# Optimization experiments

Hardware: AMD Instinct MI355X
Metric: run time of the kernel (lower is better)

The kernel has to match this reference:

```python
import jax, jax.numpy as jnp
import numpy as np

EPS = 1e-5

def mvn(x):
    # instance norm per (batch, channel) over spatial, torch var is unbiased (ddof=1)
    b, c, h, w = x.shape
    xf = x.reshape(b, c, h * w)
    mean = xf.mean(axis=2)[:, :, None, None]
    std = jnp.sqrt(jnp.var(xf, axis=2, ddof=1) + EPS)[:, :, None, None]
    return (x - mean) / std

def conv1x1(x, W, b):
    # W: [C_out, C_in], 1x1 conv == channel matmul
    return jnp.einsum('oc,bchw->bohw', W, x) + b[None, :, None, None]

def attention(Fq, G, Hs, mask_map, Wo, bo, hard):
    b, c, h, w = Fq.shape
    N = h * w
    Fm = Fq.reshape(b, c, N)          # [b,c,N]
    Gm = G.reshape(b, c, N)           # [b,c,N]
    S = jnp.einsum('bcn,bcm->bnm', Fm, Gm)  # [b,N,N] scores
    neg = -jnp.finfo(S.dtype).max
    S = jnp.where(mask_map[None, :, :] < 0.5, neg, S)
    if hard:
        # keep only the row-wise argmax entry, everything else -> neg (then softmax)
        idx = jnp.argmax(S, axis=2)                      # [b,N]
        sel = jnp.arange(N)[None, None, :] == idx[:, :, None]
        S = jnp.where(sel, S, neg)
    A = jax.nn.softmax(S, axis=-1)    # [b,N,N]
    Hm = Hs.reshape(b, c, N)
    O = jnp.einsum('bcm,bnm->bcn', Hm, A).reshape(b, c, h, w)
    return conv1x1(O, Wo, bo)

def setup_inputs() -> dict:
    key = jax.random.key(0)
    ks = jax.random.split(key, 16)
    C = 256
    shp = (2, C, 64, 64)
    inp = {
        'content': jax.random.normal(ks[0], shp, jnp.float32),
        'style': jax.random.normal(ks[1], shp, jnp.float32),
        'content_sem': jax.random.normal(ks[2], shp, jnp.float32),
        'style_sem': jax.random.normal(ks[3], shp, jnp.float32),
        'map_32': jax.random.uniform(ks[4], (1024, 1024), jnp.float32),
        'map_64': jax.random.uniform(ks[5], (4096, 4096), jnp.float32),
        't1': 1,
        't2': 1,
        'Wf': jax.random.normal(ks[6], (C, C), jnp.float32) * 0.02,
        'bf': jnp.zeros((C,), jnp.float32),
        'Wg': jax.random.normal(ks[7], (C, C), jnp.float32) * 0.02,
        'bg': jnp.zeros((C,), jnp.float32),
        'Wh': jax.random.normal(ks[8], (C, C), jnp.float32) * 0.02,
        'bh': jnp.zeros((C,), jnp.float32),
        'Wo': jax.random.normal(ks[9], (C, C), jnp.float32) * 0.02,
        'bo': jnp.zeros((C,), jnp.float32),
    }
    return inp

def reference(content, style, content_sem, style_sem, map_32, map_64, t1, t2,
              Wf, bf, Wg, bg, Wh, bh, Wo, bo):
    # h*w == 4096 -> map_64 masking branch is active (static shape decision)
    H_style = conv1x1(style, Wh, bh)
    # SCA: soft attention over semantic features
    x_sca = attention(conv1x1(mvn(content_sem), Wf, bf),
                      conv1x1(mvn(style_sem), Wg, bg),
                      H_style, map_64, Wo, bo, hard=False)
    # SSA: hard-argmax attention over content/style features
    x_ssa = attention(conv1x1(mvn(content), Wf, bf),
                      conv1x1(mvn(style), Wg, bg),
                      H_style, map_64, Wo, bo, hard=True)
    return t1 * x_sca + t2 * x_ssa + content
```

## Files before the change

kernel.cpp:

```cpp
#include <hip/hip_runtime.h>
#include <hip/hip_bf16.h>
#include <cstddef>

typedef unsigned short u16;
typedef unsigned int   u32;
typedef unsigned long long u64;
typedef short v8s __attribute__((ext_vector_type(8)));
typedef u16   v8u __attribute__((ext_vector_type(8)));
typedef float v4f __attribute__((ext_vector_type(4)));

#define CH  256
#define NSP 4096
#define NB  2

__device__ __forceinline__ float b2f(u16 u){ u32 t = ((u32)u) << 16; float f; __builtin_memcpy(&f, &t, 4); return f; }
__device__ __forceinline__ u16 f2b(float f){
  u32 x; __builtin_memcpy(&x, &f, 4);
  u32 r = x + 0x7FFFu + ((x >> 16) & 1u);
  return (u16)(r >> 16);
}
__device__ __forceinline__ u32 f2sortable(float f){
  u32 x; __builtin_memcpy(&x, &f, 4);
  return (x & 0x80000000u) ? ~x : (x | 0x80000000u);
}
__device__ __forceinline__ float sortable2f(u32 u){
  u32 x = (u & 0x80000000u) ? (u ^ 0x80000000u) : ~u;
  float f; __builtin_memcpy(&f, &x, 4);
  return f;
}

__global__ __launch_bounds__(256) void k_stats(
    const float* __restrict__ x0, const float* __restrict__ x1,
    const float* __restrict__ x2, const float* __restrict__ x3,
    float* __restrict__ meanv, float* __restrict__ rstdv){
  int bid = blockIdx.x;
  int t = bid >> 9, row = bid & 511;
  const float* src = (t==0?x0: t==1?x1: t==2?x2: x3) + (size_t)row*NSP;
  int tid = threadIdx.x;
  double sx = 0.0, sq = 0.0;
  const float4* p4 = (const float4*)src;
  #pragma unroll
  for (int k=0;k<4;k++){
    float4 v = p4[tid + k*256];
    double a=v.x,bb=v.y,c=v.z,d=v.w;
    sx += a+bb+c+d;
    sq += a*a + bb*bb + c*c + d*d;
  }
  #pragma unroll
  for (int off=1; off<64; off<<=1){ sx += __shfl_xor(sx, off); sq += __shfl_xor(sq, off); }
  __shared__ double wsx[4], wsq[4];
  int w = tid >> 6;
  if ((tid & 63) == 0){ wsx[w] = sx; wsq[w] = sq; }
  __syncthreads();
  if (tid == 0){
    double SX = wsx[0]+wsx[1]+wsx[2]+wsx[3];
    double SQ = wsq[0]+wsq[1]+wsq[2]+wsq[3];
    double mean = SX / 4096.0;
    double var  = (SQ - 4096.0*mean*mean) / 4095.0;
    double rstd = 1.0 / sqrt(var + 1e-5);
    meanv[bid] = (float)mean;
    rstdv[bid] = (float)rstd;
  }
}

__global__ __launch_bounds__(256) void k_weights(
    const float* __restrict__ Wo, const float* __restrict__ Wh,
    const float* __restrict__ bh, const float* __restrict__ bo,
    u16* __restrict__ W2, float* __restrict__ b2v){
  int o = blockIdx.x, c = threadIdx.x;
  __shared__ float wo[256];
  __shared__ float red[256];
  wo[c] = Wo[o*256 + c];
  __syncthreads();
  float acc = 0.f;
  for (int j=0;j<256;j++) acc += wo[j] * Wh[j*256 + c];
  W2[o*256 + c] = f2b(acc);
  red[c] = wo[c] * bh[c];
  __syncthreads();
  for (int s=128;s>0;s>>=1){ if (c < s) red[c] += red[c+s]; __syncthreads(); }
  if (c == 0) b2v[o] = red[0] + bo[o];
}

__global__ __launch_bounds__(256) void k_maskbits(
    const float* __restrict__ map, u32* __restrict__ bits){
  int wid = blockIdx.x*256 + threadIdx.x;
  const float4* p = (const float4*)(map + (size_t)wid*32);
  u32 m = 0;
  #pragma unroll
  for (int k=0;k<8;k++){
    float4 v = p[k];
    m |= (u32)(v.x >= 0.5f) << (k*4+0);
    m |= (u32)(v.y >= 0.5f) << (k*4+1);
    m |= (u32)(v.z >= 0.5f) << (k*4+2);
    m |= (u32)(v.w >= 0.5f) << (k*4+3);
  }
  bits[wid] = m;
}

__global__ __launch_bounds__(256,2) void k_conv_sca(
    const float* __restrict__ x, const float* __restrict__ W,
    const float* __restrict__ meanv, const float* __restrict__ rstdv, int statBase,
    const float* __restrict__ biasv, u16* __restrict__ outB){
  __shared__ u16 As[64][72];
  __shared__ u16 Bs[64][72];
  int o0 = blockIdx.x*64, n0 = blockIdx.y*64, b = blockIdx.z;
  int tid = threadIdx.x, w = tid>>6, lane = tid&63, col = lane&15, q = lane>>4;
  v4f acc[4] = {};
  int crA = tid>>2, nseg = (tid&3)*16;
  for (int kc=0; kc<4; kc++){
    int cg = kc*64;
    {
      int srow = statBase + b*256 + cg + crA;
      float mean = meanv[srow], rstd = rstdv[srow];
      const float4* xr = (const float4*)(x + ((size_t)(b*256 + cg + crA))*NSP + n0 + nseg);
      #pragma unroll
      for (int k4=0;k4<4;k4++){
        float4 v = xr[k4];
        As[nseg+k4*4+0][crA] = f2b((v.x-mean)*rstd);
        As[nseg+k4*4+1][crA] = f2b((v.y-mean)*rstd);
        As[nseg+k4*4+2][crA] = f2b((v.z-mean)*rstd);
        As[nseg+k4*4+3][crA] = f2b((v.w-mean)*rstd);
      }
    }
    {
      const float4* wr = (const float4*)(W + ((size_t)(o0 + crA))*256 + cg + nseg);
      #pragma unroll
      for (int h=0;h<2;h++){
        float4 a = wr[h*2], c = wr[h*2+1];
        v8u o;
        o[0]=f2b(a.x); o[1]=f2b(a.y); o[2]=f2b(a.z); o[3]=f2b(a.w);
        o[4]=f2b(c.x); o[5]=f2b(c.y); o[6]=f2b(c.z); o[7]=f2b(c.w);
        *(v8u*)&Bs[crA][nseg + h*8] = o;
      }
    }
    __syncthreads();
    #pragma unroll
    for (int ks=0;ks<2;ks++){
      v8s af = *(v8s*)&As[w*16 + col][ks*32 + q*8];
      #pragma unroll
      for (int js=0;js<4;js++){
        v8s bfr = *(v8s*)&Bs[js*16 + col][ks*32 + q*8];
        acc[js] = __builtin_amdgcn_mfma_f32_16x16x32_bf16(af, bfr, acc[js], 0, 0, 0);
      }
    }
    __syncthreads();
  }
  #pragma unroll
  for (int js=0;js<4;js++){
    int o = o0 + js*16 + col;
    float bj = biasv[o];
    #pragma unroll
    for (int reg=0;reg<4;reg++){
      int n = n0 + w*16 + q*4 + reg;
      outB[((size_t)(b*NSP + n))*256 + o] = f2b(acc[js][reg] + bj);
    }
  }
}

__global__ __launch_bounds__(256,2) void k_conv_ssa(
    const float* __restrict__ x, const float* __restrict__ W,
    const float* __restrict__ meanv, const float* __restrict__ rstdv, int statBase,
    const float* __restrict__ biasv,
    float* __restrict__ outF, u16* __restrict__ outB){
  __shared__ u32 As32[64][100];
  __shared__ u32 Bs32[64][100];
  int o0 = blockIdx.x*64, n0 = blockIdx.y*64, b = blockIdx.z;
  int tid = threadIdx.x, w = tid>>6, lane = tid&63, col = lane&15, q = lane>>4;
  v4f acc[4] = {};
  int cA = tid>>3, nnA = (tid&7)*8;
  int oB = tid>>2, cB = (tid&3)*8;
  for (int g=0; g<8; g++){
    int cg = g*32;
    {
      int srow = statBase + b*256 + cg + cA;
      float mean = meanv[srow], rstd = rstdv[srow];
      const float4* xr = (const float4*)(x + ((size_t)(b*256 + cg + cA))*NSP + n0 + nnA);
      float4 v0 = xr[0], v1 = xr[1];
      float xv[8] = {v0.x,v0.y,v0.z,v0.w,v1.x,v1.y,v1.z,v1.w};
      #pragma unroll
      for (int e=0;e<8;e++){
        float xm = (xv[e]-mean)*rstd;
        u16 s0 = f2b(xm);  float r1 = xm - b2f(s0);
        u16 s1 = f2b(r1);  float r2 = r1 - b2f(s1);
        u16 s2 = f2b(r2);
        As32[nnA+e][cA*3+0] = (u32)s0 | ((u32)s1<<16);
        As32[nnA+e][cA*3+1] = (u32)s2 | ((u32)s0<<16);
        As32[nnA+e][cA*3+2] = (u32)s1 | ((u32)s0<<16);
      }
    }
    {
      const float4* wr = (const float4*)(W + ((size_t)(o0 + oB))*256 + cg + cB);
      float4 w0v = wr[0], w1v = wr[1];
      float wv[8] = {w0v.x,w0v.y,w0v.z,w0v.w,w1v.x,w1v.y,w1v.z,w1v.w};
      #pragma unroll
      for (int e=0;e<8;e++){
        float ww = wv[e];
        u16 t0 = f2b(ww);  float r1 = ww - b2f(t0);
        u16 t1 = f2b(r1);  float r2 = r1 - b2f(t1);
        u16 t2 = f2b(r2);
        int cc = cB + e;
        Bs32[oB][cc*3+0] = (u32)t0 | ((u32)t0<<16);
        Bs32[oB][cc*3+1] = (u32)t0 | ((u32)t1<<16);
        Bs32[oB][cc*3+2] = (u32)t1 | ((u32)t2<<16);
      }
    }
    __syncthreads();
    #pragma unroll
    for (int ks=0;ks<6;ks++){
      v8s af = *(v8s*)&As32[w*16 + col][ks*16 + q*4];
      #pragma unroll
      for (int js=0;js<4;js++){
        v8s bfr = *(v8s*)&Bs32[js*16 + col][ks*16 + q*4];
        acc[js] = __builtin_amdgcn_mfma_f32_16x16x32_bf16(af, bfr, acc[js], 0, 0, 0);
      }
    }
    __syncthreads();
  }
  #pragma unroll
  for (int js=0;js<4;js++){
    int o = o0 + js*16 + col;
    float bj = biasv[o];
    #pragma unroll
    for (int reg=0;reg<4;reg++){
      int n = n0 + w*16 + q*4 + reg;
      float v = acc[js][reg] + bj;
      size_t idx = ((size_t)(b*NSP + n))*256 + o;
      outF[idx] = v;
      if (outB) outB[idx] = f2b(v);
    }
  }
}

__global__ __launch_bounds__(256,2) void k_vprime(
    const u16* __restrict__ w2, const float* __restrict__ style,
    const float* __restrict__ b2v, u16* __restrict__ vp){
  __shared__ u16 As[64][72];
  __shared__ u16 Bs[64][72];
  int m0 = blockIdx.x*64, o0 = blockIdx.y*64, b = blockIdx.z;
  int tid = threadIdx.x, w = tid>>6, lane = tid&63, col = lane&15, q = lane>>4;
  v4f acc[4] = {};
  for (int kc=0; kc<4; kc++){
    int cg = kc*64;
    #pragma unroll
    for (int p=0;p<2;p++){
      int id = tid + p*256;
      int row = id>>3, cc = (id&7)*8;
      *(v8s*)&As[row][cc] = *(const v8s*)(w2 + ((size_t)(o0+row))*256 + cg + cc);
    }
    {
      int cr = tid>>2, mseg = (tid&3)*16;
      const float4* sr = (const float4*)(style + ((size_t)(b*256 + cg + cr))*NSP + m0 + mseg);
      #pragma unroll
      for (int k4=0;k4<4;k4++){
        float4 v = sr[k4];
        Bs[mseg+k4*4+0][cr] = f2b(v.x);
        Bs[mseg+k4*4+1][cr] = f2b(v.y);
        Bs[mseg+k4*4+2][cr] = f2b(v.z);
        Bs[mseg+k4*4+3][cr] = f2b(v.w);
      }
    }
    __syncthreads();
    #pragma unroll
    for (int ks=0;ks<2;ks++){
      v8s af = *(v8s*)&As[w*16+col][ks*32+q*8];
      #pragma unroll
      for (int js=0;js<4;js++){
        v8s bfr = *(v8s*)&Bs[js*16+col][ks*32+q*8];
        acc[js] = __builtin_amdgcn_mfma_f32_16x16x32_bf16(af, bfr, acc[js], 0,0,0);
      }
    }
    __syncthreads();
  }
  #pragma unroll
  for (int js=0;js<4;js++){
    int m = m0 + js*16 + col;
    #pragma unroll
    for (int reg=0;reg<4;reg++){
      int o = o0 + w*16 + q*4 + reg;
      vp[((size_t)(b*CH + o))*NSP + m] = f2b(acc[js][reg] + b2v[o]);
    }
  }
}

__global__ __launch_bounds__(256,2) void k_ssa_max(
    const float* __restrict__ Qf, const u16* __restrict__ Kt,
    const u32* __restrict__ mbits, u32* __restrict__ rowmaxU){
  __shared__ u16 Ks[64][264];
  int mh = blockIdx.x, nt = blockIdx.y, b = blockIdx.z;
  int tid = threadIdx.x, w = tid>>6, lane = tid&63, col = lane&15, q = lane>>4;
  int nw = nt*64 + w*16, mbase = mh*512;
  v8s qf[8];
  const float* qrow = Qf + ((size_t)(b*NSP + nw + col))*256;
  #pragma unroll
  for (int ks=0;ks<8;ks++){
    const float4* qp = (const float4*)(qrow + ks*32 + q*8);
    float4 a = qp[0], c = qp[1];
    v8s f;
    f[0]=(short)f2b(a.x); f[1]=(short)f2b(a.y); f[2]=(short)f2b(a.z); f[3]=(short)f2b(a.w);
    f[4]=(short)f2b(c.x); f[5]=(short)f2b(c.y); f[6]=(short)f2b(c.z); f[7]=(short)f2b(c.w);
    qf[ks] = f;
  }
  float rm[4] = {-1e30f,-1e30f,-1e30f,-1e30f};
  for (int it=0; it<8; it++){
    int m0 = mbase + it*64;
    #pragma unroll
    for (int p=0;p<8;p++){
      int id = tid + p*256;
      int row = id>>5, cc = (id&31)*8;
      *(v8s*)&Ks[row][cc] = *(const v8s*)(Kt + ((size_t)(b*NSP + m0 + row))*256 + cc);
    }
    __syncthreads();
    v4f as[4] = {};
    #pragma unroll
    for (int ks=0;ks<8;ks++){
      #pragma unroll
      for (int js=0;js<4;js++){
        v8s bfr = *(v8s*)&Ks[js*16+col][ks*32+q*8];
        as[js] = __builtin_amdgcn_mfma_f32_16x16x32_bf16(qf[ks], bfr, as[js], 0, 0, 0);
      }
    }
    #pragma unroll
    for (int reg=0;reg<4;reg++){
      int ng = nw + q*4 + reg;
      u64 mw = *(const u64*)(mbits + (size_t)ng*128 + (m0>>5));
      #pragma unroll
      for (int js=0;js<4;js++){
        bool ok = (mw >> (js*16 + col)) & 1ull;
        if (ok) rm[reg] = fmaxf(rm[reg], as[js][reg]);
      }
    }
    __syncthreads();
  }
  #pragma unroll
  for (int reg=0;reg<4;reg++){
    float t = rm[reg];
    t = fmaxf(t, __shfl_xor(t,1));
    t = fmaxf(t, __shfl_xor(t,2));
    t = fmaxf(t, __shfl_xor(t,4));
    t = fmaxf(t, __shfl_xor(t,8));
    if (col == 0){
      int ng = nw + q*4 + reg;
      atomicMax(rowmaxU + (size_t)b*NSP + ng, f2sortable(t));
    }
  }
}

__global__ __launch_bounds__(256,2) void k_ssa_arg(
    const float* __restrict__ Qf, const u16* __restrict__ Kt,
    const float* __restrict__ Kf, const u32* __restrict__ mbits,
    const u32* __restrict__ rowmaxU, u64* __restrict__ argkey){
  __shared__ u16 Ks[64][264];
  int mh = blockIdx.x, nt = blockIdx.y, b = blockIdx.z;
  int tid = threadIdx.x, w = tid>>6, lane = tid&63, col = lane&15, q = lane>>4;
  int nw = nt*64 + w*16, mbase = mh*512;
  v8s qf[8];
  const float* qrow = Qf + ((size_t)(b*NSP + nw + col))*256;
  #pragma unroll
  for (int ks=0;ks<8;ks++){
    const float4* qp = (const float4*)(qrow + ks*32 + q*8);
    float4 a = qp[0], c = qp[1];
    v8s f;
    f[0]=(short)f2b(a.x); f[1]=(short)f2b(a.y); f[2]=(short)f2b(a.z); f[3]=(short)f2b(a.w);
    f[4]=(short)f2b(c.x); f[5]=(short)f2b(c.y); f[6]=(short)f2b(c.z); f[7]=(short)f2b(c.w);
    qf[ks] = f;
  }
  float thr[4];
  #pragma unroll
  for (int reg=0;reg<4;reg++){
    int ng = nw + q*4 + reg;
    thr[reg] = sortable2f(rowmaxU[(size_t)b*NSP + ng]) - 0.25f;
  }
  for (int it=0; it<8; it++){
    int m0 = mbase + it*64;
    #pragma unroll
    for (int p=0;p<8;p++){
      int id = tid + p*256;
      int row = id>>5, cc = (id&31)*8;
      *(v8s*)&Ks[row][cc] = *(const v8s*)(Kt + ((size_t)(b*NSP + m0 + row))*256 + cc);
    }
    __syncthreads();
    v4f as[4] = {};
    #pragma unroll
    for (int ks=0;ks<8;ks++){
      #pragma unroll
      for (int js=0;js<4;js++){
        v8s bfr = *(v8s*)&Ks[js*16+col][ks*32+q*8];
        as[js] = __builtin_amdgcn_mfma_f32_16x16x32_bf16(qf[ks], bfr, as[js], 0, 0, 0);
      }
    }
    #pragma unroll
    for (int reg=0;reg<4;reg++){
      int ng = nw + q*4 + reg;
      u64 mw = *(const u64*)(mbits + (size_t)ng*128 + (m0>>5));
      #pragma unroll
      for (int js=0;js<4;js++){
        int mg = m0 + js*16 + col;
        bool ok = (mw >> (js*16 + col)) & 1ull;
        if (ok && as[js][reg] >= thr[reg]){
          const float* qr = Qf + ((size_t)(b*NSP + ng))*256;
          const float* kr = Kf + ((size_t)(b*NSP + mg))*256;
          double s0=0.0, s1=0.0;
          for (int c4=0;c4<64;c4++){
            float4 av = *(const float4*)(qr + c4*4);
            float4 bv = *(const float4*)(kr + c4*4);
            s0 += (double)av.x*bv.x + (double)av.z*bv.z;
            s1 += (double)av.y*bv.y + (double)av.w*bv.w;
          }
          double dt = s0 + s1;
          u64 db; __builtin_memcpy(&db, &dt, 8);
          u64 sd = (db & 0x8000000000000000ull) ? ~db : (db | 0x8000000000000000ull);
          u64 key = (sd & ~0xFFFull) | (u64)(4095 - mg);
          atomicMax((unsigned long long*)(argkey + (size_t)b*NSP + ng), (unsigned long long)key);
        }
      }
    }
    __syncthreads();
  }
}

__global__ __launch_bounds__(256,2) void k_sca(
    const u16* __restrict__ Qt, const u16* __restrict__ Kt, const u16* __restrict__ Vp,
    const u32* __restrict__ mbits, u16* __restrict__ OpartB, float* __restrict__ lmv){
  __shared__ u16 Ks[32][264];
  __shared__ u16 Vs[256][40];
  __shared__ u16 Ps[4][16][40];
  int mh = blockIdx.x, nt = blockIdx.y, b = blockIdx.z;
  int tid = threadIdx.x, w = tid>>6, lane = tid&63, col = lane&15, q = lane>>4;
  int nw = nt*64 + w*16;
  int mbase = mh*512;
  v8s qf[8];
  const u16* qrow = Qt + ((size_t)(b*NSP + nw + col))*256;
  #pragma unroll
  for (int ks=0;ks<8;ks++) qf[ks] = *(const v8s*)(qrow + ks*32 + q*8);
  v4f ao[16] = {};
  float mr[4]   = {-1e30f,-1e30f,-1e30f,-1e30f};
  float lsum[4] = {0.f,0.f,0.f,0.f};
  for (int it=0; it<16; it++){
    int m0 = mbase + it*32;
    #pragma unroll
    for (int p=0;p<4;p++){
      int id = tid + p*256;
      int row = id>>5, cc = (id&31)*8;
      *(v8s*)&Ks[row][cc] = *(const v8s*)(Kt + ((size_t)(b*NSP + m0 + row))*256 + cc);
    }
    #pragma unroll
    for (int p=0;p<4;p++){
      int id = tid + p*256;
      int row = id>>2, cc = (id&3)*8;
      *(v8s*)&Vs[row][cc] = *(const v8s*)(Vp + ((size_t)(b*CH + row))*NSP + m0 + cc);
    }
    __syncthreads();
    v4f as[2] = {};
    #pragma unroll
    for (int ks=0;ks<8;ks++){
      #pragma unroll
      for (int js=0;js<2;js++){
        v8s bfr = *(v8s*)&Ks[js*16+col][ks*32+q*8];
        as[js] = __builtin_amdgcn_mfma_f32_16x16x32_bf16(qf[ks], bfr, as[js], 0, 0, 0);
      }
    }
    float sv[2][4];
    float tmax[4] = {-1e30f,-1e30f,-1e30f,-1e30f};
    #pragma unroll
    for (int reg=0;reg<4;reg++){
      int ng = nw + q*4 + reg;
      u32 mwrd = mbits[(size_t)ng*128 + (m0>>5)];
      #pragma unroll
      for (int js=0;js<2;js++){
        bool ok = (mwrd >> (js*16 + col)) & 1u;
        float s = ok ? as[js][reg] : -1e30f;
        sv[js][reg] = s;
        tmax[reg] = fmaxf(tmax[reg], s);
      }
    }
    float alpha[4];
    #pragma unroll
    for (int reg=0;reg<4;reg++){
      float t = tmax[reg];
      t = fmaxf(t, __shfl_xor(t,1));
      t = fmaxf(t, __shfl_xor(t,2));
      t = fmaxf(t, __shfl_xor(t,4));
      t = fmaxf(t, __shfl_xor(t,8));
      float mn = fmaxf(mr[reg], t);
      alpha[reg] = __expf(mr[reg] - mn);
      mr[reg] = mn;
    }
    float rs[4] = {0.f,0.f,0.f,0.f};
    #pragma unroll
    for (int js=0;js<2;js++){
      #pragma unroll
      for (int reg=0;reg<4;reg++){
        float s = sv[js][reg];
        float pv = (s <= -1e29f) ? 0.f : __expf(s - mr[reg]);
        Ps[w][q*4+reg][js*16+col] = f2b(pv);
        rs[reg] += pv;
      }
    }
    #pragma unroll
    for (int reg=0;reg<4;reg++){
      float r = rs[reg];
      r += __shfl_xor(r,1); r += __shfl_xor(r,2);
      r += __shfl_xor(r,4); r += __shfl_xor(r,8);
      lsum[reg] = lsum[reg]*alpha[reg] + r;
    }
    v4f al4 = {alpha[0], alpha[1], alpha[2], alpha[3]};
    #pragma unroll
    for (int os=0;os<16;os++) ao[os] *= al4;
    v8s pfr = *(v8s*)&Ps[w][col][q*8];
    #pragma unroll
    for (int os=0;os<16;os++){
      v8s vb = *(v8s*)&Vs[os*16 + col][q*8];
      ao[os] = __builtin_amdgcn_mfma_f32_16x16x32_bf16(pfr, vb, ao[os], 0, 0, 0);
    }
    __syncthreads();
  }
  size_t base = ((size_t)(mh*2 + b))*NSP;
  #pragma unroll
  for (int os=0;os<16;os++){
    #pragma unroll
    for (int reg=0;reg<4;reg++){
      int ng = nw + q*4 + reg;
      OpartB[(base + ng)*256 + os*16 + col] = f2b(ao[os][reg]);
    }
  }
  if (col == 0){
    #pragma unroll
    for (int reg=0;reg<4;reg++){
      int ng = nw + q*4 + reg;
      lmv[(base + ng)*2 + 0] = mr[reg];
      lmv[(base + ng)*2 + 1] = lsum[reg];
    }
  }
}

__global__ __launch_bounds__(256) void k_combine(
    const u16* __restrict__ OpartB, const float* __restrict__ lmv,
    const u64* __restrict__ argkey, const u16* __restrict__ Vp,
    const float* __restrict__ content, const int* __restrict__ t1p, const int* __restrict__ t2p,
    float* __restrict__ outp){
  __shared__ float T[64][65];
  __shared__ float cs[8][64];
  __shared__ int sidx[64];
  int nt = blockIdx.x, ot = blockIdx.y, b = blockIdx.z;
  int n0 = nt*64, o0 = ot*64, tid = threadIdx.x;
  float t1f = (float)t1p[0], t2f = (float)t2p[0];
  if (tid < 64){
    int ng = n0 + tid;
    u64 key = argkey[(size_t)b*NSP + ng];
    sidx[tid] = 4095 - (int)(key & 0xFFFull);
    float mp[8], lp[8];
    float M = -1e30f;
    #pragma unroll
    for (int p=0;p<8;p++){
      mp[p] = lmv[(((size_t)(p*2+b))*NSP + ng)*2 + 0];
      lp[p] = lmv[(((size_t)(p*2+b))*NSP + ng)*2 + 1];
      M = fmaxf(M, mp[p]);
    }
    float den = 0.f;
    float wv[8];
    #pragma unroll
    for (int p=0;p<8;p++){ wv[p] = __expf(mp[p] - M); den += lp[p]*wv[p]; }
    float rd = (den > 0.f) ? 1.f/den : 0.f;
    #pragma unroll
    for (int p=0;p<8;p++) cs[p][tid] = wv[p]*rd;
  }
  __syncthreads();
  int jo = tid & 63, bi = tid >> 6;
  #pragma unroll
  for (int p16=0;p16<16;p16++){
    int in_ = bi + p16*4;
    int ng = n0 + in_;
    float acc = 0.f;
    #pragma unroll
    for (int p=0;p<8;p++){
      size_t off = (((size_t)(p*2+b))*NSP + ng)*256 + o0 + jo;
      acc += b2f(OpartB[off])*cs[p][in_];
    }
    T[jo][in_] = acc;
  }
  __syncthreads();
  int nl = tid & 63, ob = tid >> 6;
  #pragma unroll
  for (int p=0;p<16;p++){
    int ol = ob + p*4;
    int og = o0 + ol;
    size_t vrow = ((size_t)(b*CH + og))*NSP;
    float v = t1f*T[ol][nl] + t2f*b2f(Vp[vrow + sidx[nl]]) + content[vrow + n0 + nl];
    outp[vrow + n0 + nl] = v;
  }
}

extern "C" void kernel_launch(void* const* d_in, const int* in_sizes, int n_in,
                              void* d_out, int out_size, void* d_ws, size_t ws_size,
                              hipStream_t stream){
  const float* content = (const float*)d_in[0];
  const float* style   = (const float*)d_in[1];
  const float* csem    = (const float*)d_in[2];
  const float* ssem    = (const float*)d_in[3];
  const float* map64   = (const float*)d_in[5];
  const int* t1p       = (const int*)d_in[6];
  const int* t2p       = (const int*)d_in[7];
  const float* Wf = (const float*)d_in[8];  const float* bfv = (const float*)d_in[9];
  const float* Wg = (const float*)d_in[10]; const float* bgv = (const float*)d_in[11];
  const float* Wh = (const float*)d_in[12]; const float* bhv = (const float*)d_in[13];
  const float* Wo = (const float*)d_in[14]; const float* bov = (const float*)d_in[15];

  char* ws = (char*)d_ws;
  size_t off = 0;
  auto alloc = [&](size_t bytes)->char*{
    char* p = ws + off;
    off += (bytes + 255) & ~(size_t)255;
    return p;
  };
  float* meanv  = (float*)alloc((size_t)4*512*4);
  float* rstdv  = (float*)alloc((size_t)4*512*4);
  float* b2v    = (float*)alloc((size_t)CH*4);
  float* lmv    = (float*)alloc((size_t)8*NB*NSP*2*4);
  u64* argkey   = (u64*)alloc((size_t)NB*NSP*8);
  u32* rowmaxU  = (u32*)alloc((size_t)NB*NSP*4);
  u16* w2       = (u16*)alloc((size_t)CH*CH*2);
  u32* mbits    = (u32*)alloc((size_t)NSP*128*4);
  u16* qt_sca   = (u16*)alloc((size_t)NB*NSP*CH*2);
  u16* kt_sca   = (u16*)alloc((size_t)NB*NSP*CH*2);
  u16* vp       = (u16*)alloc((size_t)NB*CH*NSP*2);
  char* ovl     = alloc((size_t)8*NB*NSP*CH*2);
  u16* kt_ssa   = (u16*)ovl;
  float* qff    = (float*)(ovl + (size_t)NB*NSP*CH*2);
  float* kff    = (float*)(ovl + (size_t)NB*NSP*CH*2 + (size_t)NB*NSP*CH*4);
  u16* opartB   = (u16*)ovl;
  (void)ws_size; (void)in_sizes; (void)n_in; (void)out_size;

  hipMemsetAsync(argkey, 0, (size_t)NB*NSP*8, stream);
  hipMemsetAsync(rowmaxU, 0, (size_t)NB*NSP*4, stream);

  k_stats<<<2048, 256, 0, stream>>>(csem, ssem, content, style, meanv, rstdv);
  k_weights<<<256, 256, 0, stream>>>(Wo, Wh, bhv, bov, w2, b2v);
  k_maskbits<<<2048, 256, 0, stream>>>(map64, mbits);
  k_conv_sca<<<dim3(4,64,2), 256, 0, stream>>>(csem, Wf, meanv, rstdv, 0,    bfv, qt_sca);
  k_conv_sca<<<dim3(4,64,2), 256, 0, stream>>>(ssem, Wg, meanv, rstdv, 512,  bgv, kt_sca);
  k_conv_ssa<<<dim3(4,64,2), 256, 0, stream>>>(content, Wf, meanv, rstdv, 1024, bfv, qff, nullptr);
  k_conv_ssa<<<dim3(4,64,2), 256, 0, stream>>>(style,   Wg, meanv, rstdv, 1536, bgv, kff, kt_ssa);
  k_vprime<<<dim3(64,4,2), 256, 0, stream>>>(w2, style, b2v, vp);
  k_ssa_max<<<dim3(8,64,2), 256, 0, stream>>>(qff, kt_ssa, mbits, rowmaxU);
  k_ssa_arg<<<dim3(8,64,2), 256, 0, stream>>>(qff, kt_ssa, kff, mbits, rowmaxU, argkey);
  k_sca<<<dim3(8,64,2), 256, 0, stream>>>(qt_sca, kt_sca, vp, mbits, opartB, lmv);
  k_combine<<<dim3(64,4,2), 256, 0, stream>>>(opartB, lmv, argkey, vp, content, t1p, t2p, (float*)d_out);
}
```

Before: 587.6 us.

## Materialize bf16 SSA score matrix and rescan near-max candidates in fp64

When the workspace is large enough, the hard-attention argmax path computes masked bf16 scores once per batch into a 4096x4096 buffer. A per-row scan then finds the max and re-evaluates only candidates within a small threshold in double precision. This replaces the two-pass max/argmax kernels, which recompute the full score GEMM twice and use global atomics. The cost is about 32 MB of extra write and read traffic per batch. The 0.10 threshold and the cap of 128 candidates could miss the exact argmax when bf16 rounding error is large or many entries tie.

```diff
diff --git a/kernel.cpp b/kernel.cpp
--- a/kernel.cpp
+++ b/kernel.cpp
@@ -282,6 +282,105 @@
   }
 }
 
+__global__ __launch_bounds__(256,2) void k_ssa_dump(
+    const u16* __restrict__ Qt, const u16* __restrict__ Kt,
+    const u32* __restrict__ mbits, int b, u16* __restrict__ Sb){
+  __shared__ u16 Ks[64][264];
+  int mh = blockIdx.x, nt = blockIdx.y;
+  int tid = threadIdx.x, w = tid>>6, lane = tid&63, col = lane&15, q = lane>>4;
+  int nw = nt*64 + w*16, mbase = mh*512;
+  v8s qf[8];
+  const u16* qrow = Qt + ((size_t)(b*NSP + nw + col))*256;
+  #pragma unroll
+  for (int ks=0;ks<8;ks++) qf[ks] = *(const v8s*)(qrow + ks*32 + q*8);
+  for (int it=0; it<8; it++){
+    int m0 = mbase + it*64;
+    #pragma unroll
+    for (int p=0;p<8;p++){
+      int id = tid + p*256;
+      int row = id>>5, cc = (id&31)*8;
+      *(v8s*)&Ks[row][cc] = *(const v8s*)(Kt + ((size_t)(b*NSP + m0 + row))*256 + cc);
+    }
+    __syncthreads();
+    v4f as[4] = {};
+    #pragma unroll
+    for (int ks=0;ks<8;ks++){
+      #pragma unroll
+      for (int js=0;js<4;js++){
+        v8s bfr = *(v8s*)&Ks[js*16+col][ks*32+q*8];
+        as[js] = __builtin_amdgcn_mfma_f32_16x16x32_bf16(qf[ks], bfr, as[js], 0, 0, 0);
+      }
+    }
+    #pragma unroll
+    for (int reg=0;reg<4;reg++){
+      int ng = nw + q*4 + reg;
+      u64 mw = *(const u64*)(mbits + (size_t)ng*128 + (m0>>5));
+      u16* srow = Sb + (size_t)ng*NSP + m0;
+      #pragma unroll
+      for (int js=0;js<4;js++){
+        bool ok = (mw >> (js*16 + col)) & 1ull;
+        float s = ok ? as[js][reg] : -1e30f;
+        srow[js*16 + col] = f2b(s);
+      }
+    }
+    __syncthreads();
+  }
+}
+
+__global__ __launch_bounds__(256) void k_ssa_scan(
+    const u16* __restrict__ Sb, const float* __restrict__ Qf, const float* __restrict__ Kf,
+    int b, int* __restrict__ argidx){
+  int wv = threadIdx.x >> 6, lane = threadIdx.x & 63;
+  int n = blockIdx.x*4 + wv;
+  const u16* srow = Sb + (size_t)n*NSP;
+  v8u sv[8];
+  #pragma unroll
+  for (int j=0;j<4;j++){
+    const v8u* p = (const v8u*)(srow + j*1024 + lane*16);
+    sv[j*2]   = p[0];
+    sv[j*2+1] = p[1];
+  }
+  float smax = -3e38f;
+  #pragma unroll
+  for (int r=0;r<8;r++){
+    #pragma unroll
+    for (int e=0;e<8;e++) smax = fmaxf(smax, b2f(sv[r][e]));
+  }
+  smax = fmaxf(smax, __shfl_xor(smax,1));
+  smax = fmaxf(smax, __shfl_xor(smax,2));
+  smax = fmaxf(smax, __shfl_xor(smax,4));
+  smax = fmaxf(smax, __shfl_xor(smax,8));
+  smax = fmaxf(smax, __shfl_xor(smax,16));
+  smax = fmaxf(smax, __shfl_xor(smax,32));
+  int bmg = 0;
+  if (smax > -1e29f){
+    float thr = smax - 0.10f;
+    float4 q4 = *(const float4*)(Qf + ((size_t)(b*NSP + n))*256 + lane*4);
+    double bd = -1e308;
+    bmg = -1;
+    int cand = 0;
+    for (int j=0;j<4;j++){
+      for (int e=0;e<16;e++){
+        float sval = b2f(sv[j*2 + (e>>3)][e&7]);
+        u64 bl = __ballot(sval >= thr);
+        while (bl && cand < 128){
+          int l2 = __builtin_ctzll(bl);
+          bl &= bl - 1;
+          cand++;
+          int mg = j*1024 + l2*16 + e;
+          float4 k4 = *(const float4*)(Kf + ((size_t)(b*NSP + mg))*256 + lane*4);
+          double d = (double)q4.x*k4.x + (double)q4.y*k4.y + (double)q4.z*k4.z + (double)q4.w*k4.w;
+          d += __shfl_xor(d,1); d += __shfl_xor(d,2); d += __shfl_xor(d,4);
+          d += __shfl_xor(d,8); d += __shfl_xor(d,16); d += __shfl_xor(d,32);
+          if (d > bd || (d == bd && mg < bmg)){ bd = d; bmg = mg; }
+        }
+      }
+    }
+    if (bmg < 0) bmg = 0;
+  }
+  if (lane == 0) argidx[b*NSP + n] = bmg;
+}
+
 __global__ __launch_bounds__(256,2) void k_ssa_max(
     const float* __restrict__ Qf, const u16* __restrict__ Kt,
     const u32* __restrict__ mbits, u32* __restrict__ rowmaxU){
@@ -418,6 +517,14 @@
   }
 }
 
+__global__ __launch_bounds__(256) void k_key2idx(const u64* __restrict__ argkey, int* __restrict__ argidx){
+  int i = blockIdx.x*256 + threadIdx.x;
+  if (i < NB*NSP){
+    u64 key = argkey[i];
+    argidx[i] = 4095 - (int)(key & 0xFFFull);
+  }
+}
+
 __global__ __launch_bounds__(256,2) void k_sca(
     const u16* __restrict__ Qt, const u16* __restrict__ Kt, const u16* __restrict__ Vp,
     const u32* __restrict__ mbits, u16* __restrict__ OpartB, float* __restrict__ lmv){
@@ -535,7 +642,7 @@
 
 __global__ __launch_bounds__(256) void k_combine(
     const u16* __restrict__ OpartB, const float* __restrict__ lmv,
-    const u64* __restrict__ argkey, const u16* __restrict__ Vp,
+    const int* __restrict__ argidx, const u16* __restrict__ Vp,
     const float* __restrict__ content, const int* __restrict__ t1p, const int* __restrict__ t2p,
     float* __restrict__ outp){
   __shared__ float T[64][65];
@@ -546,8 +653,7 @@
   float t1f = (float)t1p[0], t2f = (float)t2p[0];
   if (tid < 64){
     int ng = n0 + tid;
-    u64 key = argkey[(size_t)b*NSP + ng];
-    sidx[tid] = 4095 - (int)(key & 0xFFFull);
+    sidx[tid] = argidx[b*NSP + ng] & 4095;
     float mp[8], lp[8];
     float M = -1e30f;
     #pragma unroll
@@ -618,17 +724,23 @@
   float* lmv    = (float*)alloc((size_t)8*NB*NSP*2*4);
   u64* argkey   = (u64*)alloc((size_t)NB*NSP*8);
   u32* rowmaxU  = (u32*)alloc((size_t)NB*NSP*4);
+  int* argidx   = (int*)alloc((size_t)NB*NSP*4);
   u16* w2       = (u16*)alloc((size_t)CH*CH*2);
   u32* mbits    = (u32*)alloc((size_t)NSP*128*4);
   u16* qt_sca   = (u16*)alloc((size_t)NB*NSP*CH*2);
   u16* kt_sca   = (u16*)alloc((size_t)NB*NSP*CH*2);
   u16* vp       = (u16*)alloc((size_t)NB*CH*NSP*2);
+  u16* qt_ssa   = (u16*)alloc((size_t)NB*NSP*CH*2);
   char* ovl     = alloc((size_t)8*NB*NSP*CH*2);
   u16* kt_ssa   = (u16*)ovl;
   float* qff    = (float*)(ovl + (size_t)NB*NSP*CH*2);
   float* kff    = (float*)(ovl + (size_t)NB*NSP*CH*2 + (size_t)NB*NSP*CH*4);
   u16* opartB   = (u16*)ovl;
-  (void)ws_size; (void)in_sizes; (void)n_in; (void)out_size;
+  size_t base_need = off;
+  u16* Sb       = (u16*)alloc((size_t)NSP*NSP*2);
+  size_t full_need = off;
+  bool bigws = (ws_size >= full_need);
+  (void)in_sizes; (void)n_in; (void)out_size; (void)base_need;
 
   hipMemsetAsync(argkey, 0, (size_t)NB*NSP*8, stream);
   hipMemsetAsync(rowmaxU, 0, (size_t)NB*NSP*4, stream);
@@ -638,11 +750,19 @@
   k_maskbits<<<2048, 256, 0, stream>>>(map64, mbits);
   k_conv_sca<<<dim3(4,64,2), 256, 0, stream>>>(csem, Wf, meanv, rstdv, 0,    bfv, qt_sca);
   k_conv_sca<<<dim3(4,64,2), 256, 0, stream>>>(ssem, Wg, meanv, rstdv, 512,  bgv, kt_sca);
-  k_conv_ssa<<<dim3(4,64,2), 256, 0, stream>>>(content, Wf, meanv, rstdv, 1024, bfv, qff, nullptr);
+  k_conv_ssa<<<dim3(4,64,2), 256, 0, stream>>>(content, Wf, meanv, rstdv, 1024, bfv, qff, qt_ssa);
   k_conv_ssa<<<dim3(4,64,2), 256, 0, stream>>>(style,   Wg, meanv, rstdv, 1536, bgv, kff, kt_ssa);
   k_vprime<<<dim3(64,4,2), 256, 0, stream>>>(w2, style, b2v, vp);
-  k_ssa_max<<<dim3(8,64,2), 256, 0, stream>>>(qff, kt_ssa, mbits, rowmaxU);
-  k_ssa_arg<<<dim3(8,64,2), 256, 0, stream>>>(qff, kt_ssa, kff, mbits, rowmaxU, argkey);
+  if (bigws){
+    for (int b=0;b<2;b++){
+      k_ssa_dump<<<dim3(8,64,1), 256, 0, stream>>>(qt_ssa, kt_ssa, mbits, b, Sb);
+      k_ssa_scan<<<1024, 256, 0, stream>>>(Sb, qff, kff, b, argidx);
+    }
+  } else {
+    k_ssa_max<<<dim3(8,64,2), 256, 0, stream>>>(qff, kt_ssa, mbits, rowmaxU);
+    k_ssa_arg<<<dim3(8,64,2), 256, 0, stream>>>(qff, kt_ssa, kff, mbits, rowmaxU, argkey);
+    k_key2idx<<<32, 256, 0, stream>>>(argkey, argidx);
+  }
   k_sca<<<dim3(8,64,2), 256, 0, stream>>>(qt_sca, kt_sca, vp, mbits, opartB, lmv);
-  k_combine<<<dim3(64,4,2), 256, 0, stream>>>(opartB, lmv, argkey, vp, content, t1p, t2p, (float*)d_out);
-}
+  k_combine<<<dim3(64,4,2), 256, 0, stream>>>(opartB, lmv, argidx, vp, content, t1p, t2p, (float*)d_out);
+}
```

Result: slower. 1.462 ms (+148.9%).

## Replace two-pass SSA argmax with single-pass score dump and selective exact resolve

Applied to the files above, without the earlier changes.

The hard-attention argmax no longer runs two full QK passes (max, then threshold plus exact recompute). A single pass writes bf16 scores to a scratch matrix and tracks the top-two values and first index per row. Rows where the top two are clearly separated take that index directly. Ambiguous rows go on a worklist, and a resolve kernel rescans the stored scores and recomputes candidates in double precision. This removes one full MFMA pass, at the cost of a 32MB score write per batch, per-batch serialized launches, and a cap of 128 candidates per row in the resolve step.

```diff
diff --git a/kernel.cpp b/kernel.cpp
--- a/kernel.cpp
+++ b/kernel.cpp
@@ -18,15 +18,6 @@
   u32 x; __builtin_memcpy(&x, &f, 4);
   u32 r = x + 0x7FFFu + ((x >> 16) & 1u);
   return (u16)(r >> 16);
-}
-__device__ __forceinline__ u32 f2sortable(float f){
-  u32 x; __builtin_memcpy(&x, &f, 4);
-  return (x & 0x80000000u) ? ~x : (x | 0x80000000u);
-}
-__device__ __forceinline__ float sortable2f(u32 u){
-  u32 x = (u & 0x80000000u) ? (u ^ 0x80000000u) : ~u;
-  float f; __builtin_memcpy(&f, &x, 4);
-  return f;
 }
 
 __global__ __launch_bounds__(256) void k_stats(
@@ -282,25 +273,21 @@
   }
 }
 
-__global__ __launch_bounds__(256,2) void k_ssa_max(
-    const float* __restrict__ Qf, const u16* __restrict__ Kt,
-    const u32* __restrict__ mbits, u32* __restrict__ rowmaxU){
+__global__ __launch_bounds__(256,2) void k_ssa_dump3(
+    const u16* __restrict__ Qt, const u16* __restrict__ Kt,
+    const u32* __restrict__ mbits, int b, u16* __restrict__ Sb,
+    float2* __restrict__ pt, int* __restrict__ pi){
   __shared__ u16 Ks[64][264];
-  int mh = blockIdx.x, nt = blockIdx.y, b = blockIdx.z;
+  int mh = blockIdx.x, nt = blockIdx.y;
   int tid = threadIdx.x, w = tid>>6, lane = tid&63, col = lane&15, q = lane>>4;
   int nw = nt*64 + w*16, mbase = mh*512;
   v8s qf[8];
-  const float* qrow = Qf + ((size_t)(b*NSP + nw + col))*256;
-  #pragma unroll
-  for (int ks=0;ks<8;ks++){
-    const float4* qp = (const float4*)(qrow + ks*32 + q*8);
-    float4 a = qp[0], c = qp[1];
-    v8s f;
-    f[0]=(short)f2b(a.x); f[1]=(short)f2b(a.y); f[2]=(short)f2b(a.z); f[3]=(short)f2b(a.w);
-    f[4]=(short)f2b(c.x); f[5]=(short)f2b(c.y); f[6]=(short)f2b(c.z); f[7]=(short)f2b(c.w);
-    qf[ks] = f;
-  }
-  float rm[4] = {-1e30f,-1e30f,-1e30f,-1e30f};
+  const u16* qrow = Qt + ((size_t)(b*NSP + nw + col))*256;
+  #pragma unroll
+  for (int ks=0;ks<8;ks++) qf[ks] = *(const v8s*)(qrow + ks*32 + q*8);
+  float t1[4] = {-1e30f,-1e30f,-1e30f,-1e30f};
+  float t2[4] = {-1e30f,-1e30f,-1e30f,-1e30f};
+  int   i1[4] = {0,0,0,0};
   for (int it=0; it<8; it++){
     int m0 = mbase + it*64;
     #pragma unroll
@@ -323,99 +310,113 @@
     for (int reg=0;reg<4;reg++){
       int ng = nw + q*4 + reg;
       u64 mw = *(const u64*)(mbits + (size_t)ng*128 + (m0>>5));
-      #pragma unroll
-      for (int js=0;js<4;js++){
-        bool ok = (mw >> (js*16 + col)) & 1ull;
-        if (ok) rm[reg] = fmaxf(rm[reg], as[js][reg]);
-      }
-    }
-    __syncthreads();
-  }
-  #pragma unroll
-  for (int reg=0;reg<4;reg++){
-    float t = rm[reg];
-    t = fmaxf(t, __shfl_xor(t,1));
-    t = fmaxf(t, __shfl_xor(t,2));
-    t = fmaxf(t, __shfl_xor(t,4));
-    t = fmaxf(t, __shfl_xor(t,8));
-    if (col == 0){
-      int ng = nw + q*4 + reg;
-      atomicMax(rowmaxU + (size_t)b*NSP + ng, f2sortable(t));
-    }
-  }
-}
-
-__global__ __launch_bounds__(256,2) void k_ssa_arg(
-    const float* __restrict__ Qf, const u16* __restrict__ Kt,
-    const float* __restrict__ Kf, const u32* __restrict__ mbits,
-    const u32* __restrict__ rowmaxU, u64* __restrict__ argkey){
-  __shared__ u16 Ks[64][264];
-  int mh = blockIdx.x, nt = blockIdx.y, b = blockIdx.z;
-  int tid = threadIdx.x, w = tid>>6, lane = tid&63, col = lane&15, q = lane>>4;
-  int nw = nt*64 + w*16, mbase = mh*512;
-  v8s qf[8];
-  const float* qrow = Qf + ((size_t)(b*NSP + nw + col))*256;
-  #pragma unroll
-  for (int ks=0;ks<8;ks++){
-    const float4* qp = (const float4*)(qrow + ks*32 + q*8);
-    float4 a = qp[0], c = qp[1];
-    v8s f;
-    f[0]=(short)f2b(a.x); f[1]=(short)f2b(a.y); f[2]=(short)f2b(a.z); f[3]=(short)f2b(a.w);
-    f[4]=(short)f2b(c.x); f[5]=(short)f2b(c.y); f[6]=(short)f2b(c.z); f[7]=(short)f2b(c.w);
-    qf[ks] = f;
-  }
-  float thr[4];
-  #pragma unroll
-  for (int reg=0;reg<4;reg++){
-    int ng = nw + q*4 + reg;
-    thr[reg] = sortable2f(rowmaxU[(size_t)b*NSP + ng]) - 0.25f;
-  }
-  for (int it=0; it<8; it++){
-    int m0 = mbase + it*64;
-    #pragma unroll
-    for (int p=0;p<8;p++){
-      int id = tid + p*256;
-      int row = id>>5, cc = (id&31)*8;
-      *(v8s*)&Ks[row][cc] = *(const v8s*)(Kt + ((size_t)(b*NSP + m0 + row))*256 + cc);
-    }
-    __syncthreads();
-    v4f as[4] = {};
-    #pragma unroll
-    for (int ks=0;ks<8;ks++){
-      #pragma unroll
-      for (int js=0;js<4;js++){
-        v8s bfr = *(v8s*)&Ks[js*16+col][ks*32+q*8];
-        as[js] = __builtin_amdgcn_mfma_f32_16x16x32_bf16(qf[ks], bfr, as[js], 0, 0, 0);
-      }
-    }
-    #pragma unroll
-    for (int reg=0;reg<4;reg++){
-      int ng = nw + q*4 + reg;
-      u64 mw = *(const u64*)(mbits + (size_t)ng*128 + (m0>>5));
+      u16* srow = Sb + (size_t)ng*NSP + m0;
       #pragma unroll
       for (int js=0;js<4;js++){
         int mg = m0 + js*16 + col;
         bool ok = (mw >> (js*16 + col)) & 1ull;
-        if (ok && as[js][reg] >= thr[reg]){
-          const float* qr = Qf + ((size_t)(b*NSP + ng))*256;
-          const float* kr = Kf + ((size_t)(b*NSP + mg))*256;
-          double s0=0.0, s1=0.0;
-          for (int c4=0;c4<64;c4++){
-            float4 av = *(const float4*)(qr + c4*4);
-            float4 bv = *(const float4*)(kr + c4*4);
-            s0 += (double)av.x*bv.x + (double)av.z*bv.z;
-            s1 += (double)av.y*bv.y + (double)av.w*bv.w;
-          }
-          double dt = s0 + s1;
-          u64 db; __builtin_memcpy(&db, &dt, 8);
-          u64 sd = (db & 0x8000000000000000ull) ? ~db : (db | 0x8000000000000000ull);
-          u64 key = (sd & ~0xFFFull) | (u64)(4095 - mg);
-          atomicMax((unsigned long long*)(argkey + (size_t)b*NSP + ng), (unsigned long long)key);
+        float s = ok ? as[js][reg] : -1e30f;
+        u16 sh = f2b(s);
+        float sb = b2f(sh);
+        srow[js*16 + col] = sh;
+        if (sb > t1[reg]){ t2[reg] = t1[reg]; t1[reg] = sb; i1[reg] = mg; }
+        else {
+          if (sb == t1[reg] && mg < i1[reg]) i1[reg] = mg;
+          t2[reg] = fmaxf(t2[reg], sb);
         }
       }
     }
     __syncthreads();
   }
+  #pragma unroll
+  for (int reg=0;reg<4;reg++){
+    #pragma unroll
+    for (int off=1; off<16; off<<=1){
+      float o1 = __shfl_xor(t1[reg], off);
+      int   oi = __shfl_xor(i1[reg], off);
+      float o2 = __shfl_xor(t2[reg], off);
+      if (o1 > t1[reg]){ t2[reg] = fmaxf(t1[reg], o2); t1[reg] = o1; i1[reg] = oi; }
+      else if (o1 == t1[reg]){ i1[reg] = min(i1[reg], oi); t2[reg] = t1[reg]; }
+      else { t2[reg] = fmaxf(t2[reg], o1); }
+    }
+    if (col == 0){
+      int ng = nw + q*4 + reg;
+      pt[(size_t)mh*NSP + ng] = make_float2(t1[reg], t2[reg]);
+      pi[mh*NSP + ng] = i1[reg];
+    }
+  }
+}
+
+__global__ __launch_bounds__(256) void k_ssa_merge(
+    const float2* __restrict__ pt, const int* __restrict__ pi,
+    int b, float* __restrict__ rowmaxF, int* __restrict__ argidx,
+    int* __restrict__ wl, int* __restrict__ wlc){
+  int ng = blockIdx.x*256 + threadIdx.x;
+  float t1 = -3e38f, t2 = -3e38f; int i1 = 0;
+  #pragma unroll
+  for (int p=0;p<8;p++){
+    float2 o = pt[(size_t)p*NSP + ng];
+    int oi = pi[p*NSP + ng];
+    if (o.x > t1){ t2 = fmaxf(t1, o.y); t1 = o.x; i1 = oi; }
+    else if (o.x == t1){ i1 = min(i1, oi); t2 = t1; }
+    else { t2 = fmaxf(t2, o.x); }
+  }
+  rowmaxF[b*NSP + ng] = t1;
+  if (t1 - t2 > 0.10f){
+    argidx[b*NSP + ng] = i1;
+  } else {
+    int slot = atomicAdd(wlc, 1);
+    wl[slot] = ng;
+  }
+}
+
+__global__ __launch_bounds__(256) void k_ssa_resolve(
+    const u16* __restrict__ Sb, const float* __restrict__ Qf, const float* __restrict__ Kf,
+    const float* __restrict__ rowmaxF, const int* __restrict__ wl, const int* __restrict__ wlc,
+    int b, int* __restrict__ argidx){
+  int wv = threadIdx.x >> 6, lane = threadIdx.x & 63;
+  int cnt = wlc[0];
+  int slot = blockIdx.x*4 + wv;
+  if (slot >= cnt) return;
+  int n = wl[slot];
+  float rmx = rowmaxF[b*NSP + n];
+  int bmg = 0;
+  if (rmx > -1e29f){
+    const u16* srow = Sb + (size_t)n*NSP;
+    v8u sv[8];
+    #pragma unroll
+    for (int j=0;j<4;j++){
+      const v8u* p = (const v8u*)(srow + j*1024 + lane*16);
+      sv[j*2]   = p[0];
+      sv[j*2+1] = p[1];
+    }
+    float thr = rmx - 0.10f;
+    float4 q4 = *(const float4*)(Qf + ((size_t)(b*NSP + n))*256 + lane*4);
+    double bd = -1e308;
+    bmg = -1;
+    int cand = 0;
+    #pragma unroll
+    for (int j=0;j<4;j++){
+      #pragma unroll
+      for (int e=0;e<16;e++){
+        float sval = b2f(sv[j*2 + (e>>3)][e&7]);
+        u64 bl = __ballot(sval >= thr);
+        while (bl && cand < 128){
+          int l2 = __builtin_ctzll(bl);
+          bl &= bl - 1;
+          cand++;
+          int mg = j*1024 + l2*16 + e;
+          float4 k4 = *(const float4*)(Kf + ((size_t)(b*NSP + mg))*256 + lane*4);
+          double d = (double)q4.x*k4.x + (double)q4.y*k4.y + (double)q4.z*k4.z + (double)q4.w*k4.w;
+          d += __shfl_xor(d,1); d += __shfl_xor(d,2); d += __shfl_xor(d,4);
+          d += __shfl_xor(d,8); d += __shfl_xor(d,16); d += __shfl_xor(d,32);
+          if (d > bd || (d == bd && mg < bmg)){ bd = d; bmg = mg; }
+        }
+      }
+    }
+    if (bmg < 0) bmg = 0;
+  }
+  if (lane == 0) argidx[b*NSP + n] = bmg;
 }
 
 __global__ __launch_bounds__(256,2) void k_sca(
@@ -535,7 +536,7 @@
 
 __global__ __launch_bounds__(256) void k_combine(
     const u16* __restrict__ OpartB, const float* __restrict__ lmv,
-    const u64* __restrict__ argkey, const u16* __restrict__ Vp,
+    const int* __restrict__ argidx, const u16* __restrict__ Vp,
     const float* __restrict__ content, const int* __restrict__ t1p, const int* __restrict__ t2p,
     float* __restrict__ outp){
   __shared__ float T[64][65];
@@ -546,8 +547,7 @@
   float t1f = (float)t1p[0], t2f = (float)t2p[0];
   if (tid < 64){
     int ng = n0 + tid;
-    u64 key = argkey[(size_t)b*NSP + ng];
-    sidx[tid] = 4095 - (int)(key & 0xFFFull);
+    sidx[tid] = argidx[b*NSP + ng] & 4095;
     float mp[8], lp[8];
     float M = -1e30f;
     #pragma unroll
@@ -616,33 +616,41 @@
   float* rstdv  = (float*)alloc((size_t)4*512*4);
   float* b2v    = (float*)alloc((size_t)CH*4);
   float* lmv    = (float*)alloc((size_t)8*NB*NSP*2*4);
-  u64* argkey   = (u64*)alloc((size_t)NB*NSP*8);
-  u32* rowmaxU  = (u32*)alloc((size_t)NB*NSP*4);
+  float* rowmaxF= (float*)alloc((size_t)NB*NSP*4);
+  int* argidx   = (int*)alloc((size_t)NB*NSP*4);
+  int* wl       = (int*)alloc((size_t)NB*NSP*4);
+  int* wlc      = (int*)alloc((size_t)NB*4);
+  float2* pt    = (float2*)alloc((size_t)8*NSP*8);
+  int* pi       = (int*)alloc((size_t)8*NSP*4);
   u16* w2       = (u16*)alloc((size_t)CH*CH*2);
   u32* mbits    = (u32*)alloc((size_t)NSP*128*4);
   u16* qt_sca   = (u16*)alloc((size_t)NB*NSP*CH*2);
   u16* kt_sca   = (u16*)alloc((size_t)NB*NSP*CH*2);
   u16* vp       = (u16*)alloc((size_t)NB*CH*NSP*2);
+  u16* qt_ssa   = (u16*)alloc((size_t)NB*NSP*CH*2);
   char* ovl     = alloc((size_t)8*NB*NSP*CH*2);
   u16* kt_ssa   = (u16*)ovl;
   float* qff    = (float*)(ovl + (size_t)NB*NSP*CH*2);
   float* kff    = (float*)(ovl + (size_t)NB*NSP*CH*2 + (size_t)NB*NSP*CH*4);
   u16* opartB   = (u16*)ovl;
-  (void)ws_size; (void)in_sizes; (void)n_in; (void)out_size;
-
-  hipMemsetAsync(argkey, 0, (size_t)NB*NSP*8, stream);
-  hipMemsetAsync(rowmaxU, 0, (size_t)NB*NSP*4, stream);
+  u16* Sb       = (u16*)alloc((size_t)NSP*NSP*2);
+  (void)in_sizes; (void)n_in; (void)out_size; (void)ws_size;
+
+  hipMemsetAsync(wlc, 0, (size_t)NB*4, stream);
 
   k_stats<<<2048, 256, 0, stream>>>(csem, ssem, content, style, meanv, rstdv);
   k_weights<<<256, 256, 0, stream>>>(Wo, Wh, bhv, bov, w2, b2v);
   k_maskbits<<<2048, 256, 0, stream>>>(map64, mbits);
   k_conv_sca<<<dim3(4,64,2), 256, 0, stream>>>(csem, Wf, meanv, rstdv, 0,    bfv, qt_sca);
   k_conv_sca<<<dim3(4,64,2), 256, 0, stream>>>(ssem, Wg, meanv, rstdv, 512,  bgv, kt_sca);
-  k_conv_ssa<<<dim3(4,64,2), 256, 0, stream>>>(content, Wf, meanv, rstdv, 1024, bfv, qff, nullptr);
+  k_conv_ssa<<<dim3(4,64,2), 256, 0, stream>>>(content, Wf, meanv, rstdv, 1024, bfv, qff, qt_ssa);
   k_conv_ssa<<<dim3(4,64,2), 256, 0, stream>>>(style,   Wg, meanv, rstdv, 1536, bgv, kff, kt_ssa);
   k_vprime<<<dim3(64,4,2), 256, 0, stream>>>(w2, style, b2v, vp);
-  k_ssa_max<<<dim3(8,64,2), 256, 0, stream>>>(qff, kt_ssa, mbits, rowmaxU);
-  k_ssa_arg<<<dim3(8,64,2), 256, 0, stream>>>(qff, kt_ssa, kff, mbits, rowmaxU, argkey);
+  for (int b=0;b<2;b++){
+    k_ssa_dump3<<<dim3(8,64,1), 256, 0, stream>>>(qt_ssa, kt_ssa, mbits, b, Sb, pt, pi);
+    k_ssa_merge<<<16, 256, 0, stream>>>(pt, pi, b, rowmaxF, argidx, wl + b*NSP, wlc + b);
+    k_ssa_resolve<<<1024, 256, 0, stream>>>(Sb, qff, kff, rowmaxF, wl + b*NSP, wlc + b, b, argidx);
+  }
   k_sca<<<dim3(8,64,2), 256, 0, stream>>>(qt_sca, kt_sca, vp, mbits, opartB, lmv);
-  k_combine<<<dim3(64,4,2), 256, 0, stream>>>(opartB, lmv, argkey, vp, content, t1p, t2p, (float*)d_out);
-}
+  k_combine<<<dim3(64,4,2), 256, 0, stream>>>(opartB, lmv, argidx, vp, content, t1p, t2p, (float*)d_out);
+}
```

Result: faster. 493.1 us (-16.1%).
